# Performance work log

Hardware: AMD Instinct MI355X
Metric: run time of the kernel (lower is better)

The kernel has to match this reference:

```python
import jax, jax.numpy as jnp
import numpy as np

B, F, D, R, U = 65536, 8, 2, 10, 32  # batch, leaves, local_dim, rank, units


def setup_inputs() -> dict:
    key = jax.random.key(0)
    ks = jax.random.split(key, 9)
    s = 0.3  # glorot-ish scale for tiny tensors
    return {
        "X": jax.random.normal(ks[0], (B, F, D), dtype=jnp.float32),
        "core11": jax.random.normal(ks[1], (R, R, R), dtype=jnp.float32) * s,
        "core12": jax.random.normal(ks[2], (R, R, R), dtype=jnp.float32) * s,
        "core13": jax.random.normal(ks[3], (R, R, R), dtype=jnp.float32) * s,
        "core14": jax.random.normal(ks[4], (R, R, R), dtype=jnp.float32) * s,
        "core21": jax.random.normal(ks[5], (R, R, R), dtype=jnp.float32) * s,
        "core22": jax.random.normal(ks[6], (R, R, R), dtype=jnp.float32) * s,
        "factor_matrices": jax.random.normal(ks[7], (D, R, F, U), dtype=jnp.float32) * s,
        "matrix_top": jax.random.normal(ks[8], (R, R), dtype=jnp.float32) * s,
    }


def _pair(a, b, core):
    # con[j] = sum_{i,k} a[i] * b[k] * core[i,k,j]  (per unit u, batch b)
    return jnp.einsum('ubi,ubk,ikj->ubj', a, b, core)


def reference(X, core11, core12, core13, core14, core21, core22,
              factor_matrices, matrix_top):
    # leaf contraction over local_dim, all units at once: [F, U, B, R]
    c = jnp.einsum('bfd,drfu->fubr', X, factor_matrices)
    # level 1 of the tree (pairs of leaves)
    p1 = _pair(c[0], c[1], core11)
    p2 = _pair(c[2], c[3], core12)
    p3 = _pair(c[4], c[5], core13)
    p4 = _pair(c[6], c[7], core14)
    # level 2
    q1 = _pair(p1, p2, core21)
    q2 = _pair(p3, p4, core22)
    # top: (q1 @ matrix_top) . q2 -> scalar per (unit, batch); activation is linear
    out = jnp.einsum('ubi,ij,ubj->bu', q1, matrix_top, q2)
    return out  # [B, U]
```

## Files before the change

kernel.cpp:

```cpp
#include <hip/hip_runtime.h>


#define BB 65536
#define FF 8
#define DD 2
#define RR 10
#define UU 32

typedef __attribute__((ext_vector_type(8))) short short8;
typedef __attribute__((ext_vector_type(4))) float f32x4;
typedef __attribute__((ext_vector_type(4))) unsigned int u32x4;

__device__ __forceinline__ unsigned short f2bf_trunc(float x) {
    return (unsigned short)(__builtin_bit_cast(unsigned int, x) >> 16);
}
__device__ __forceinline__ float bf2f(unsigned short h) {
    return __builtin_bit_cast(float, ((unsigned int)h) << 16);
}
__device__ __forceinline__ unsigned int bcu(float x) {
    return __builtin_bit_cast(unsigned int, x);
}
__device__ __forceinline__ float bcf(unsigned int x) {
    return __builtin_bit_cast(float, x);
}


__global__ __launch_bounds__(256) void precompute_T_fast(
    const float* __restrict__ core11, const float* __restrict__ core12,
    const float* __restrict__ core13, const float* __restrict__ core14,
    const float* __restrict__ core21, const float* __restrict__ core22,
    const float* __restrict__ FM, const float* __restrict__ MT,
    unsigned short* __restrict__ Thi, unsigned short* __restrict__ Tlo)
{
    const int u   = blockIdx.x;
    const int tid = threadIdx.x;

    __shared__ float sC[6][RR * RR * RR];
    __shared__ float sMT[RR * RR];
    __shared__ float sLeaf[FF][2][RR];
    __shared__ float sP[4][4][RR];
    __shared__ float sQ[2][16][RR];
    __shared__ float sR1[16][RR];

#pragma unroll
    for (int r = 0; r < 4; ++r) {
        const int o = tid + 256 * r;
        if (o < RR * RR * RR) {
            sC[0][o] = core11[o];
            sC[1][o] = core12[o];
            sC[2][o] = core13[o];
            sC[3][o] = core14[o];
            sC[4][o] = core21[o];
            sC[5][o] = core22[o];
        }
    }
    if (tid < RR * RR) sMT[tid] = MT[tid];

    if (tid < FF * 2 * RR) {
        const int f = tid / (2 * RR);
        const int rem = tid % (2 * RR);
        const int a = rem / RR;
        const int r = rem % RR;
        sLeaf[f][a][r] = FM[((a * RR + r) * FF + f) * UU + u];
    }
    __syncthreads();

    if (tid < 4 * 4 * RR) {
        const int P   = tid / (4 * RR);
        const int rem = tid % (4 * RR);
        const int s   = rem / RR;
        const int j   = rem % RR;
        const int fa = 2 * P, fb = 2 * P + 1;
        const int ai = s & 1, bi = s >> 1;
        const float* cp = sC[P];
        float a[RR], b[RR];
#pragma unroll
        for (int i = 0; i < RR; ++i) { a[i] = sLeaf[fa][ai][i]; b[i] = sLeaf[fb][bi][i]; }
        float acc0 = 0.0f, acc1 = 0.0f;
#pragma unroll
        for (int i = 0; i < RR; ++i) {
#pragma unroll
            for (int k = 0; k < RR; ++k) {
                const float w = a[i] * b[k];
                const float c = cp[(i * RR + k) * RR + j];
                if (i & 1) acc1 = fmaf(w, c, acc1);
                else       acc0 = fmaf(w, c, acc0);
            }
        }
        sP[P][s][j] = acc0 + acc1;
    }
    __syncthreads();

    for (int t = tid; t < 2 * 16 * RR; t += 256) {
        const int side  = t / (16 * RR);
        const int rem   = t % (16 * RR);
        const int combo = rem / RR;
        const int j     = rem % RR;
        const int pa = side * 2, pb = side * 2 + 1;
        const float* cp = sC[4 + side];
        float a[RR], b[RR];
#pragma unroll
        for (int i = 0; i < RR; ++i) {
            a[i] = sP[pa][combo & 3][i];
            b[i] = sP[pb][combo >> 2][i];
        }
        float acc0 = 0.0f, acc1 = 0.0f;
#pragma unroll
        for (int i = 0; i < RR; ++i) {
#pragma unroll
            for (int k = 0; k < RR; ++k) {
                const float w = a[i] * b[k];
                const float c = cp[(i * RR + k) * RR + j];
                if (i & 1) acc1 = fmaf(w, c, acc1);
                else       acc0 = fmaf(w, c, acc0);
            }
        }
        sQ[side][combo][j] = acc0 + acc1;
    }
    __syncthreads();

    if (tid < 16 * RR) {
        const int p = tid / RR;
        const int j = tid % RR;
        float acc = 0.0f;
#pragma unroll
        for (int i = 0; i < RR; ++i)
            acc = fmaf(sQ[0][p][i], sMT[i * RR + j], acc);
        sR1[p][j] = acc;
    }
    __syncthreads();

    {
        const int c = tid;
        const int p = c & 15, q = c >> 4;
        float acc = 0.0f;
#pragma unroll
        for (int j = 0; j < RR; ++j)
            acc = fmaf(sR1[p][j], sQ[1][q][j], acc);
        const unsigned short h = f2bf_trunc(acc);
        const unsigned short l = f2bf_trunc(acc - bf2f(h));
        Thi[u * 256 + c] = h;
        Tlo[u * 256 + c] = l;
    }
}


#define NWAVE 1024
#define ITER  4

__global__ __launch_bounds__(256, 2) void tree_eval_mfma(
    const float* __restrict__ X,
    const unsigned short* __restrict__ Thi,
    const unsigned short* __restrict__ Tlo,
    float* __restrict__ out)
{
    const int lane  = threadIdx.x & 63;
    const int wid   = threadIdx.x >> 6;
    const int gw    = blockIdx.x * 4 + wid;
    const int ubase = blockIdx.y * 16;

    const int n  = lane & 15;
    const int kb = lane >> 4;

    const unsigned short* th = Thi + (ubase + n) * 256 + kb * 8;
    const unsigned short* tl = Tlo + (ubase + n) * 256 + kb * 8;
    short8 bh[8], bl[8];
#pragma unroll
    for (int s = 0; s < 8; ++s) {
        bh[s] = *reinterpret_cast<const short8*>(th + s * 32);
        bl[s] = *reinterpret_cast<const short8*>(tl + s * 32);
    }

    const int qpar = kb >> 1;
    const int kpar = kb & 1;

#pragma unroll
    for (int it = 0; it < ITER; ++it) {
        const int bbase = (it * NWAVE + gw) * 16;

        const float* xp = X + (size_t)(bbase + n) * (FF * DD);
        const float4 v0 = *reinterpret_cast<const float4*>(xp + 0);
        const float4 v1 = *reinterpret_cast<const float4*>(xp + 4);
        const float4 v2 = *reinterpret_cast<const float4*>(xp + 8);
        const float4 v3 = *reinterpret_cast<const float4*>(xp + 12);

        float t01[4], t23[4], t45[4], t67[4];
        t01[0] = v0.x * v0.z; t01[1] = v0.y * v0.z; t01[2] = v0.x * v0.w; t01[3] = v0.y * v0.w;
        t23[0] = v1.x * v1.z; t23[1] = v1.y * v1.z; t23[2] = v1.x * v1.w; t23[3] = v1.y * v1.w;
        t45[0] = v2.x * v2.z; t45[1] = v2.y * v2.z; t45[2] = v2.x * v2.w; t45[3] = v2.y * v2.w;
        t67[0] = v3.x * v3.z; t67[1] = v3.y * v3.z; t67[2] = v3.x * v3.w; t67[3] = v3.y * v3.w;

        const float v23_0 = kpar ? t23[2] : t23[0];
        const float v23_1 = kpar ? t23[3] : t23[1];
        float w1own[8];
#pragma unroll
        for (int j = 0; j < 8; ++j)
            w1own[j] = t01[j & 3] * ((j >> 2) ? v23_1 : v23_0);

        const float u45_0 = qpar ? t45[1] : t45[0];
        const float u45_1 = qpar ? t45[3] : t45[2];

        f32x4 acc0 = {0.0f, 0.0f, 0.0f, 0.0f};
        f32x4 acc1 = {0.0f, 0.0f, 0.0f, 0.0f};
        f32x4 acc2 = {0.0f, 0.0f, 0.0f, 0.0f};

#pragma unroll
        for (int s = 0; s < 8; ++s) {
            const float w2s = ((s & 1) ? u45_1 : u45_0) * t67[s >> 1];

            u32x4 ahp, alp;
#pragma unroll
            for (int e = 0; e < 4; ++e) {
                const float a0 = w1own[2 * e + 0] * w2s;
                const float a1 = w1own[2 * e + 1] * w2s;
                ahp[e] = __builtin_amdgcn_perm(bcu(a1), bcu(a0), 0x07060302u);
                const float r0 = a0 - bcf(bcu(a0) & 0xFFFF0000u);
                const float r1 = a1 - bcf(bcu(a1) & 0xFFFF0000u);
                alp[e] = __builtin_amdgcn_perm(bcu(r1), bcu(r0), 0x07060302u);
            }
            const short8 ah = __builtin_bit_cast(short8, ahp);
            const short8 al = __builtin_bit_cast(short8, alp);

            acc0 = __builtin_amdgcn_mfma_f32_16x16x32_bf16(ah, bh[s], acc0, 0, 0, 0);
            acc1 = __builtin_amdgcn_mfma_f32_16x16x32_bf16(al, bh[s], acc1, 0, 0, 0);
            acc2 = __builtin_amdgcn_mfma_f32_16x16x32_bf16(ah, bl[s], acc2, 0, 0, 0);
        }

        float* op = out + (size_t)(bbase + kb * 4) * UU + ubase + n;
#pragma unroll
        for (int r = 0; r < 4; ++r)
            op[(size_t)r * UU] = (acc0[r] + acc1[r]) + acc2[r];
    }
}

extern "C" void kernel_launch(void* const* d_in, const int* in_sizes, int n_in,
                              void* d_out, int out_size, void* d_ws, size_t ws_size,
                              hipStream_t stream) {
    const float* X      = (const float*)d_in[0];
    const float* core11 = (const float*)d_in[1];
    const float* core12 = (const float*)d_in[2];
    const float* core13 = (const float*)d_in[3];
    const float* core14 = (const float*)d_in[4];
    const float* core21 = (const float*)d_in[5];
    const float* core22 = (const float*)d_in[6];
    const float* FM     = (const float*)d_in[7];
    const float* MT     = (const float*)d_in[8];
    float* out          = (float*)d_out;

    unsigned short* Thi = (unsigned short*)d_ws;
    unsigned short* Tlo = Thi + UU * 256;

    precompute_T_fast<<<dim3(UU), dim3(256), 0, stream>>>(
        core11, core12, core13, core14, core21, core22, FM, MT, Thi, Tlo);

    tree_eval_mfma<<<dim3(256, 2), dim3(256), 0, stream>>>(X, Thi, Tlo, out);
}
```

Before: 84.44 us.

## Fuse T precompute and tree evaluation into one cooperative kernel with grid sync

Merges the per-unit T precompute kernel and the MFMA evaluation kernel into a single cooperative launch. The first 32 blocks compute T, a grid-wide sync follows, and then every block runs evaluation with 512 threads covering both unit halves. The aim is to remove the second kernel launch and the gap between the two kernels. In exchange it adds a grid barrier, and every block waits on the slowest precompute block.

```diff
diff --git a/kernel.cpp b/kernel.cpp
--- a/kernel.cpp
+++ b/kernel.cpp
@@ -1,5 +1,8 @@
 #include <hip/hip_runtime.h>
-
+#include <hip/hip_cooperative_groups.h>
+
+
+namespace cg = cooperative_groups;
 
 #define BB 65536
 #define FF 8
@@ -24,16 +27,20 @@
     return __builtin_bit_cast(float, x);
 }
 
-
-__global__ __launch_bounds__(256) void precompute_T_fast(
+#define NWAVE 1024
+#define ITER  4
+
+__global__ __launch_bounds__(512, 2) void fused_tree(
+    const float* __restrict__ X,
     const float* __restrict__ core11, const float* __restrict__ core12,
     const float* __restrict__ core13, const float* __restrict__ core14,
     const float* __restrict__ core21, const float* __restrict__ core22,
     const float* __restrict__ FM, const float* __restrict__ MT,
-    unsigned short* __restrict__ Thi, unsigned short* __restrict__ Tlo)
+    unsigned short* __restrict__ Thi, unsigned short* __restrict__ Tlo,
+    float* __restrict__ out)
 {
-    const int u   = blockIdx.x;
     const int tid = threadIdx.x;
+    const int bid = blockIdx.x;
 
     __shared__ float sC[6][RR * RR * RR];
     __shared__ float sMT[RR * RR];
@@ -42,122 +49,117 @@
     __shared__ float sQ[2][16][RR];
     __shared__ float sR1[16][RR];
 
-#pragma unroll
-    for (int r = 0; r < 4; ++r) {
-        const int o = tid + 256 * r;
-        if (o < RR * RR * RR) {
-            sC[0][o] = core11[o];
-            sC[1][o] = core12[o];
-            sC[2][o] = core13[o];
-            sC[3][o] = core14[o];
-            sC[4][o] = core21[o];
-            sC[5][o] = core22[o];
+    if (bid < UU) {
+        const int u = bid;
+
+#pragma unroll
+        for (int r = 0; r < 2; ++r) {
+            const int o = tid + 512 * r;
+            if (o < RR * RR * RR) {
+                sC[0][o] = core11[o];
+                sC[1][o] = core12[o];
+                sC[2][o] = core13[o];
+                sC[3][o] = core14[o];
+                sC[4][o] = core21[o];
+                sC[5][o] = core22[o];
+            }
+        }
+        if (tid < RR * RR) sMT[tid] = MT[tid];
+
+        if (tid < FF * 2 * RR) {
+            const int f = tid / (2 * RR);
+            const int rem = tid % (2 * RR);
+            const int a = rem / RR;
+            const int r = rem % RR;
+            sLeaf[f][a][r] = FM[((a * RR + r) * FF + f) * UU + u];
+        }
+        __syncthreads();
+
+        if (tid < 4 * 4 * RR) {
+            const int P   = tid / (4 * RR);
+            const int rem = tid % (4 * RR);
+            const int s   = rem / RR;
+            const int j   = rem % RR;
+            const int fa = 2 * P, fb = 2 * P + 1;
+            const int ai = s & 1, bi = s >> 1;
+            const float* cp = sC[P];
+            float a[RR], b[RR];
+#pragma unroll
+            for (int i = 0; i < RR; ++i) { a[i] = sLeaf[fa][ai][i]; b[i] = sLeaf[fb][bi][i]; }
+            float acc0 = 0.0f, acc1 = 0.0f;
+#pragma unroll
+            for (int i = 0; i < RR; ++i) {
+#pragma unroll
+                for (int k = 0; k < RR; ++k) {
+                    const float w = a[i] * b[k];
+                    const float c = cp[(i * RR + k) * RR + j];
+                    if (i & 1) acc1 = fmaf(w, c, acc1);
+                    else       acc0 = fmaf(w, c, acc0);
+                }
+            }
+            sP[P][s][j] = acc0 + acc1;
+        }
+        __syncthreads();
+
+        if (tid < 2 * 16 * RR) {
+            const int side  = tid / (16 * RR);
+            const int rem   = tid % (16 * RR);
+            const int combo = rem / RR;
+            const int j     = rem % RR;
+            const int pa = side * 2, pb = side * 2 + 1;
+            const float* cp = sC[4 + side];
+            float a[RR], b[RR];
+#pragma unroll
+            for (int i = 0; i < RR; ++i) {
+                a[i] = sP[pa][combo & 3][i];
+                b[i] = sP[pb][combo >> 2][i];
+            }
+            float acc0 = 0.0f, acc1 = 0.0f;
+#pragma unroll
+            for (int i = 0; i < RR; ++i) {
+#pragma unroll
+                for (int k = 0; k < RR; ++k) {
+                    const float w = a[i] * b[k];
+                    const float c = cp[(i * RR + k) * RR + j];
+                    if (i & 1) acc1 = fmaf(w, c, acc1);
+                    else       acc0 = fmaf(w, c, acc0);
+                }
+            }
+            sQ[side][combo][j] = acc0 + acc1;
+        }
+        __syncthreads();
+
+        if (tid < 16 * RR) {
+            const int p = tid / RR;
+            const int j = tid % RR;
+            float acc = 0.0f;
+#pragma unroll
+            for (int i = 0; i < RR; ++i)
+                acc = fmaf(sQ[0][p][i], sMT[i * RR + j], acc);
+            sR1[p][j] = acc;
+        }
+        __syncthreads();
+
+        if (tid < 256) {
+            const int c = tid;
+            const int p = c & 15, q = c >> 4;
+            float acc = 0.0f;
+#pragma unroll
+            for (int j = 0; j < RR; ++j)
+                acc = fmaf(sR1[p][j], sQ[1][q][j], acc);
+            const unsigned short h = f2bf_trunc(acc);
+            const unsigned short l = f2bf_trunc(acc - bf2f(h));
+            Thi[u * 256 + c] = h;
+            Tlo[u * 256 + c] = l;
         }
     }
-    if (tid < RR * RR) sMT[tid] = MT[tid];
-
-    if (tid < FF * 2 * RR) {
-        const int f = tid / (2 * RR);
-        const int rem = tid % (2 * RR);
-        const int a = rem / RR;
-        const int r = rem % RR;
-        sLeaf[f][a][r] = FM[((a * RR + r) * FF + f) * UU + u];
-    }
-    __syncthreads();
-
-    if (tid < 4 * 4 * RR) {
-        const int P   = tid / (4 * RR);
-        const int rem = tid % (4 * RR);
-        const int s   = rem / RR;
-        const int j   = rem % RR;
-        const int fa = 2 * P, fb = 2 * P + 1;
-        const int ai = s & 1, bi = s >> 1;
-        const float* cp = sC[P];
-        float a[RR], b[RR];
-#pragma unroll
-        for (int i = 0; i < RR; ++i) { a[i] = sLeaf[fa][ai][i]; b[i] = sLeaf[fb][bi][i]; }
-        float acc0 = 0.0f, acc1 = 0.0f;
-#pragma unroll
-        for (int i = 0; i < RR; ++i) {
-#pragma unroll
-            for (int k = 0; k < RR; ++k) {
-                const float w = a[i] * b[k];
-                const float c = cp[(i * RR + k) * RR + j];
-                if (i & 1) acc1 = fmaf(w, c, acc1);
-                else       acc0 = fmaf(w, c, acc0);
-            }
-        }
-        sP[P][s][j] = acc0 + acc1;
-    }
-    __syncthreads();
-
-    for (int t = tid; t < 2 * 16 * RR; t += 256) {
-        const int side  = t / (16 * RR);
-        const int rem   = t % (16 * RR);
-        const int combo = rem / RR;
-        const int j     = rem % RR;
-        const int pa = side * 2, pb = side * 2 + 1;
-        const float* cp = sC[4 + side];
-        float a[RR], b[RR];
-#pragma unroll
-        for (int i = 0; i < RR; ++i) {
-            a[i] = sP[pa][combo & 3][i];
-            b[i] = sP[pb][combo >> 2][i];
-        }
-        float acc0 = 0.0f, acc1 = 0.0f;
-#pragma unroll
-        for (int i = 0; i < RR; ++i) {
-#pragma unroll
-            for (int k = 0; k < RR; ++k) {
-                const float w = a[i] * b[k];
-                const float c = cp[(i * RR + k) * RR + j];
-                if (i & 1) acc1 = fmaf(w, c, acc1);
-                else       acc0 = fmaf(w, c, acc0);
-            }
-        }
-        sQ[side][combo][j] = acc0 + acc1;
-    }
-    __syncthreads();
-
-    if (tid < 16 * RR) {
-        const int p = tid / RR;
-        const int j = tid % RR;
-        float acc = 0.0f;
-#pragma unroll
-        for (int i = 0; i < RR; ++i)
-            acc = fmaf(sQ[0][p][i], sMT[i * RR + j], acc);
-        sR1[p][j] = acc;
-    }
-    __syncthreads();
-
-    {
-        const int c = tid;
-        const int p = c & 15, q = c >> 4;
-        float acc = 0.0f;
-#pragma unroll
-        for (int j = 0; j < RR; ++j)
-            acc = fmaf(sR1[p][j], sQ[1][q][j], acc);
-        const unsigned short h = f2bf_trunc(acc);
-        const unsigned short l = f2bf_trunc(acc - bf2f(h));
-        Thi[u * 256 + c] = h;
-        Tlo[u * 256 + c] = l;
-    }
-}
-
-
-#define NWAVE 1024
-#define ITER  4
-
-__global__ __launch_bounds__(256, 2) void tree_eval_mfma(
-    const float* __restrict__ X,
-    const unsigned short* __restrict__ Thi,
-    const unsigned short* __restrict__ Tlo,
-    float* __restrict__ out)
-{
-    const int lane  = threadIdx.x & 63;
-    const int wid   = threadIdx.x >> 6;
-    const int gw    = blockIdx.x * 4 + wid;
-    const int ubase = blockIdx.y * 16;
+
+    cg::this_grid().sync();
+
+    const int lane  = tid & 63;
+    const int wid   = tid >> 6;
+    const int gw    = bid * 4 + (wid & 3);
+    const int ubase = (wid >> 2) * 16;
 
     const int n  = lane & 15;
     const int kb = lane >> 4;
@@ -250,8 +252,14 @@
     unsigned short* Thi = (unsigned short*)d_ws;
     unsigned short* Tlo = Thi + UU * 256;
 
-    precompute_T_fast<<<dim3(UU), dim3(256), 0, stream>>>(
-        core11, core12, core13, core14, core21, core22, FM, MT, Thi, Tlo);
-
-    tree_eval_mfma<<<dim3(256, 2), dim3(256), 0, stream>>>(X, Thi, Tlo, out);
-}
+    void* args[] = {
+        (void*)&X,
+        (void*)&core11, (void*)&core12, (void*)&core13, (void*)&core14,
+        (void*)&core21, (void*)&core22,
+        (void*)&FM, (void*)&MT,
+        (void*)&Thi, (void*)&Tlo,
+        (void*)&out
+    };
+    hipLaunchCooperativeKernel((void*)fused_tree, dim3(256), dim3(512),
+                               args, 0, stream);
+}
```

Result: slower. 127.3 us (+50.7%).
